# Kernel tuning notes

Hardware: AMD Instinct MI355X
Metric: run time of the kernel (lower is better)

The kernel has to match this reference:

```python
import jax, jax.numpy as jnp
import numpy as np

B, T, C, H = 4, 2048, 1024, 16
D = C // H  # head dim = 64
ROPE_BASE = 10000.0


def _rope_cache(seq_len, dim, dtype=jnp.float32):
    # torchtune-style interleaved RoPE cache
    inv_freq = 1.0 / (ROPE_BASE ** (jnp.arange(0, dim, 2, dtype=jnp.float32) / dim))
    t = jnp.arange(seq_len, dtype=jnp.float32)
    freqs = jnp.outer(t, inv_freq)  # [T, D/2]
    return jnp.cos(freqs).astype(dtype), jnp.sin(freqs).astype(dtype)


def _apply_rope(x, cos, sin):
    # x: [B, H, T, D]; rotate interleaved pairs along last dim
    x1 = x[..., 0::2]
    x2 = x[..., 1::2]
    # broadcast cos/sin [T, D/2] -> [1, 1, T, D/2]
    o1 = x1 * cos - x2 * sin
    o2 = x2 * cos + x1 * sin
    out = jnp.stack([o1, o2], axis=-1).reshape(x.shape)
    return out


def setup_inputs() -> dict:
    key = jax.random.key(0)
    k1, k2, k3 = jax.random.split(key, 3)
    x = jax.random.normal(k1, (B, T, C), dtype=jnp.float32)
    W_in = jax.random.normal(k2, (C, 3 * C), dtype=jnp.float32) * (1.0 / np.sqrt(C))
    b_in = jnp.zeros((3 * C,), dtype=jnp.float32)
    W_out = jax.random.normal(k3, (C, C), dtype=jnp.float32) * (1.0 / np.sqrt(C))
    b_out = jnp.zeros((C,), dtype=jnp.float32)
    return {"x": x, "W_in": W_in, "b_in": b_in, "W_out": W_out, "b_out": b_out}


def reference(x, W_in, b_in, W_out, b_out):
    Bx, Tx, Cx = x.shape
    qkv = x @ W_in + b_in                      # [B, T, 3C]
    q, k, v = jnp.split(qkv, 3, axis=-1)
    # [B, T, C] -> [B, H, T, D]
    def to_heads(t):
        return t.reshape(Bx, Tx, H, D).transpose(0, 2, 1, 3)
    q, k, v = to_heads(q), to_heads(k), to_heads(v)

    cos, sin = _rope_cache(Tx, D, dtype=x.dtype)
    q = _apply_rope(q, cos, sin)
    k = _apply_rope(k, cos, sin)

    scale = 1.0 / np.sqrt(D)
    att = jnp.einsum('bhqd,bhkd->bhqk', q, k) * scale   # [B, H, T, T]
    causal = jnp.tril(jnp.ones((Tx, Tx), dtype=bool))
    att = jnp.where(causal[None, None, :, :], att, jnp.float32(-jnp.inf).astype(att.dtype))
    att = jax.nn.softmax(att, axis=-1)
    # dropout = 0.0 (eval mode): identity
    y = jnp.einsum('bhqk,bhkd->bhqd', att, v)           # [B, H, T, D]
    y = y.transpose(0, 2, 1, 3).reshape(Bx, Tx, Cx)     # [B, T, C]
    return y @ W_out + b_out
```

## Files before the change

kernel.cpp:

```cpp
#include <hip/hip_runtime.h>

#define B_ 4
#define T_ 2048
#define C_ 1024
#define H_ 16
#define D_ 64
#define M_ (B_*T_)
#define N3_ (3*C_)
#define NKT_ 32

typedef unsigned short u16;
typedef short bf16x8 __attribute__((ext_vector_type(8)));
typedef short bf16x4 __attribute__((ext_vector_type(4)));
typedef unsigned short u16x8 __attribute__((ext_vector_type(8)));
typedef unsigned int u32x4 __attribute__((ext_vector_type(4)));
typedef float f32x4 __attribute__((ext_vector_type(4)));
typedef float f32x16 __attribute__((ext_vector_type(16)));

#define QSCALE 0.18033688f
#define DEFER_THR 11.0f

__device__ __forceinline__ u16 f2bf(float f) {
  unsigned u = __float_as_uint(f);
  u += 0x7fffu + ((u >> 16) & 1u);
  return (u16)(u >> 16);
}
__device__ __forceinline__ float bf2f(u16 u) { return __uint_as_float(((unsigned)u) << 16); }

__device__ __forceinline__ unsigned cvt_pk_bf16(float lo, float hi) {
  unsigned r;
  asm("v_cvt_pk_bf16_f32 %0, %1, %2" : "=v"(r) : "v"(lo), "v"(hi));
  return r;
}

__device__ __forceinline__ void gload16(const void* g, void* l) {
  __builtin_amdgcn_global_load_lds((const __attribute__((address_space(1))) void*)g,
                                   (__attribute__((address_space(3))) void*)l, 16, 0, 0);
}

__global__ __launch_bounds__(256) void k_convert(const float* __restrict__ in,
                                                 u16* __restrict__ out, int n8) {
  int i = blockIdx.x * 256 + threadIdx.x;
  if (i >= n8) return;
  f32x4 a = *(const f32x4*)(in + (size_t)i * 8);
  f32x4 b = *(const f32x4*)(in + (size_t)i * 8 + 4);
  u16x8 o;
  #pragma unroll
  for (int j = 0; j < 4; ++j) { o[j] = f2bf(a[j]); o[4 + j] = f2bf(b[j]); }
  *(u16x8*)(out + (size_t)i * 8) = o;
}

__global__ __launch_bounds__(256) void k_transpose(const float* __restrict__ W,
                                                   u16* __restrict__ Wt, int K, int N) {
  __shared__ float tile[64][65];
  int n0 = blockIdx.x * 64, k0 = blockIdx.y * 64;
  int c = threadIdx.x & 63, r0 = threadIdx.x >> 6;
  #pragma unroll
  for (int i = 0; i < 16; ++i) {
    int r = i * 4 + r0;
    tile[r][c] = W[(size_t)(k0 + r) * N + n0 + c];
  }
  __syncthreads();
  #pragma unroll
  for (int i = 0; i < 16; ++i) {
    int r = i * 4 + r0;
    Wt[(size_t)(n0 + r) * K + k0 + c] = f2bf(tile[c][r]);
  }
}

__global__ void k_rope_table(float* __restrict__ ct, float* __restrict__ st) {
  int idx = blockIdx.x * 256 + threadIdx.x;
  int t = idx >> 5, i = idx & 31;
  double inv = exp(-(2.0 * (double)i / 64.0) * log(10000.0));
  double a = (double)t * inv;
  ct[idx] = (float)cos(a);
  st[idx] = (float)sin(a);
}

__global__ __launch_bounds__(256) void k_vtrans(const u16* __restrict__ V,
                                                u16* __restrict__ Vt) {
  __shared__ u16 tile[64][65];
  int t0 = blockIdx.x * 64;
  size_t bh = (size_t)blockIdx.z * H_ + blockIdx.y;
  const u16* src = V + (bh * T_ + t0) * D_;
  u16* dst = Vt + bh * (size_t)D_ * T_ + t0;
  int r0 = threadIdx.x >> 3, c0 = (threadIdx.x & 7) * 8;
  #pragma unroll
  for (int i = 0; i < 2; ++i) {
    int rr = i * 32 + r0;
    u16x8 v = *(const u16x8*)(src + rr * D_ + c0);
    #pragma unroll
    for (int j = 0; j < 8; ++j) tile[rr][c0 + j] = v[j];
  }
  __syncthreads();
  #pragma unroll
  for (int i = 0; i < 2; ++i) {
    int d = i * 32 + r0;
    u16x8 o;
    #pragma unroll
    for (int j = 0; j < 8; ++j) o[j] = tile[c0 + j][d];
    *(u16x8*)(dst + (size_t)d * T_ + c0) = o;
  }
}

template <int MODE>
__global__ __launch_bounds__(256) void k_gemm(const u16* __restrict__ A,
                                              const u16* __restrict__ Bt,
                                              const float* __restrict__ bias,
                                              float* __restrict__ Cout,
                                              u16* __restrict__ Qb, u16* __restrict__ Kb,
                                              u16* __restrict__ Vb,
                                              const float* __restrict__ ctab,
                                              const float* __restrict__ stab,
                                              int Md, int Nd, int Kd) {
  __shared__ u16 sAB[2][128 * 64];
  u16* sA = sAB[0];
  u16* sB = sAB[1];
  const int tid = threadIdx.x, lane = tid & 63, w = tid >> 6;
  const int g = lane >> 4, r = lane & 15;
  const int wm = w >> 1, wn = w & 1;
  const int lin = blockIdx.y * gridDim.x + blockIdx.x;
  const int tM = ((lin & 7) * 8 + ((lin >> 3) & 7)) * 128;
  const int tN = (lin >> 6) * 128;

  f32x4 acc[4][4];
  #pragma unroll
  for (int i = 0; i < 4; ++i)
    #pragma unroll
    for (int j = 0; j < 4; ++j) acc[i][j] = (f32x4){0.f, 0.f, 0.f, 0.f};

  for (int k0 = 0; k0 < Kd; k0 += 64) {
    #pragma unroll
    for (int i = 0; i < 4; ++i) {
      int c = i * 256 + tid, row = c >> 3, slot = (c & 7) ^ (row & 7);
      gload16(A + (size_t)(tM + row) * Kd + k0 + slot * 8, sA + (i * 256 + w * 64) * 8);
    }
    #pragma unroll
    for (int i = 0; i < 4; ++i) {
      int c = i * 256 + tid, row = c >> 3, slot = (c & 7) ^ (row & 7);
      gload16(Bt + (size_t)(tN + row) * Kd + k0 + slot * 8, sB + (i * 256 + w * 64) * 8);
    }
    __syncthreads();
    bf16x8 af[4][2], bfr[4][2];
    #pragma unroll
    for (int mt = 0; mt < 4; ++mt)
      #pragma unroll
      for (int kk = 0; kk < 2; ++kk) {
        int row = wm * 64 + mt * 16 + r;
        af[mt][kk] = *(const bf16x8*)(sA + ((row * 64 + kk * 32 + g * 8) ^ ((row & 7) << 3)));
      }
    #pragma unroll
    for (int nt = 0; nt < 4; ++nt)
      #pragma unroll
      for (int kk = 0; kk < 2; ++kk) {
        int row = wn * 64 + nt * 16 + r;
        bfr[nt][kk] = *(const bf16x8*)(sB + ((row * 64 + kk * 32 + g * 8) ^ ((row & 7) << 3)));
      }
    __builtin_amdgcn_s_setprio(1);
    #pragma unroll
    for (int mt = 0; mt < 4; ++mt)
      #pragma unroll
      for (int nt = 0; nt < 4; ++nt)
        #pragma unroll
        for (int kk = 0; kk < 2; ++kk)
          acc[mt][nt] = __builtin_amdgcn_mfma_f32_16x16x32_bf16(af[mt][kk], bfr[nt][kk],
                                                                acc[mt][nt], 0, 0, 0);
    __builtin_amdgcn_s_setprio(0);
    __syncthreads();
  }

  if (MODE == 1) {
    #pragma unroll
    for (int mt = 0; mt < 4; ++mt)
      #pragma unroll
      for (int nt = 0; nt < 4; ++nt) {
        int n = tN + wn * 64 + nt * 16 + r;
        float bv = bias[n];
        #pragma unroll
        for (int reg = 0; reg < 4; ++reg) {
          int m = tM + wm * 64 + mt * 16 + g * 4 + reg;
          Cout[(size_t)m * Nd + n] = acc[mt][nt][reg] + bv;
        }
      }
  } else {
    u16* tile = &sAB[0][0];
    #pragma unroll
    for (int mt = 0; mt < 4; ++mt)
      #pragma unroll
      for (int nt = 0; nt < 4; ++nt) {
        int nl = wn * 64 + nt * 16 + r;
        int n = tN + nl;
        float bv = bias[n];
        int sec = n >> 10, dd = n & 63;
        #pragma unroll
        for (int reg = 0; reg < 4; ++reg) {
          int ml = wm * 64 + mt * 16 + g * 4 + reg;
          int tt = (tM + ml) & (T_ - 1);
          float v = acc[mt][nt][reg] + bv;
          if (sec < 2) {
            float pv = __shfl_xor(v, 1);
            int pi = tt * 32 + (dd >> 1);
            float c = ctab[pi], sn = stab[pi];
            v = (dd & 1) ? (v * c + pv * sn) : (v * c - pv * sn);
            if (sec == 0) v *= QSCALE;
          }
          tile[ml * 128 + ((((nl >> 3) ^ (ml & 7)) << 3) | (nl & 7))] = f2bf(v);
        }
      }
    __syncthreads();
    #pragma unroll
    for (int i = 0; i < 8; ++i) {
      int row = w * 32 + (i & 3) * 8 + (lane >> 3);
      int cc = (i >> 2) * 8 + (lane & 7);
      u16x8 val = *(const u16x8*)(tile + row * 128 + ((cc ^ (row & 7)) << 3));
      int n = tN + cc * 8;
      int m = tM + row;
      int sec = n >> 10, idx = n & 1023, hh = idx >> 6, dd = idx & 63;
      int bb = m >> 11, tt = m & (T_ - 1);
      size_t off = ((size_t)(bb * H_ + hh) * T_ + tt) * D_ + dd;
      u16* dst = sec == 0 ? Qb : (sec == 1 ? Kb : Vb);
      *(u16x8*)(dst + off) = val;
    }
  }
}

__global__ __launch_bounds__(128) void k_attn(const u16* __restrict__ Qb,
                                              const u16* __restrict__ Kb,
                                              const u16* __restrict__ Vt,
                                              u16* __restrict__ Y) {
  __shared__ u16 sK[2][64 * 64];
  __shared__ u16 sV[2][64 * 64];
  const int tid = threadIdx.x, w = tid >> 6;
  const int lane = tid & 63, col = lane & 31, hi = lane >> 5;
  const int pair = blockIdx.x;
  const int h = blockIdx.y, b = blockIdx.z;
  const size_t bhK = ((size_t)b * H_ + h) * T_;
  const size_t bhV = ((size_t)b * H_ + h) * D_;

  const int qtA = pair, qtB = (NKT_ - 1) - pair;
  const int ntA = qtA + 1;
  const int total = NKT_ + 1;

  auto STAGE = [&](int buf, int kt) {
    #pragma unroll
    for (int i = 0; i < 4; ++i) {
      int c = i * 128 + tid, row = c >> 3, slot = (c & 7) ^ (row & 7);
      gload16(Kb + (bhK + kt * 64 + row) * D_ + slot * 8, &sK[buf][(i * 128 + w * 64) * 8]);
    }
    #pragma unroll
    for (int i = 0; i < 4; ++i) {
      int c = i * 128 + tid, row = c >> 3, slot = (c & 7) ^ (row & 7);
      gload16(Vt + (bhV + row) * T_ + kt * 64 + slot * 8, &sV[buf][(i * 128 + w * 64) * 8]);
    }
  };

  int qw = qtA * 64 + w * 32;
  int tq = qw + col;
  bf16x8 qf[4];
  #pragma unroll
  for (int c = 0; c < 4; ++c)
    qf[c] = *(const bf16x8*)(Qb + (bhK + tq) * D_ + c * 16 + hi * 8);

  float m_run = -3e38f, l_run = 0.f;
  f32x16 o0, o1;
  #pragma unroll
  for (int i = 0; i < 16; ++i) { o0[i] = 0.f; o1[i] = 0.f; }

  auto FINAL = [&]() {
    float lr = l_run + __shfl_xor(l_run, 32);
    float rl = 1.0f / lr;
    u16* yrow = Y + ((size_t)b * T_ + tq) * C_ + h * 64;
    #pragma unroll
    for (int dt = 0; dt < 2; ++dt)
      #pragma unroll
      for (int j = 0; j < 8; ++j) {
        float a0 = (dt ? o1[2 * j] : o0[2 * j]) * rl;
        float a1 = (dt ? o1[2 * j + 1] : o0[2 * j + 1]) * rl;
        int d = dt * 32 + 8 * (j >> 1) + 4 * hi + 2 * (j & 1);
        *(unsigned*)(yrow + d) = cvt_pk_bf16(a0, a1);
      }
  };

  STAGE(0, 0);
  __syncthreads();

  for (int it = 0; it < total; ++it) {
    const int cur = it & 1;
    if (it + 1 < total) {
      int nit = it + 1;
      STAGE(cur ^ 1, nit < ntA ? nit : nit - ntA);
    }
    const int ktl = it < ntA ? it : it - ntA;
    const int kb = ktl * 64;
    if (kb <= qw + 31) {
      const bool act1 = (kb + 32 <= qw + 31);
      f32x16 s0, s1;
      #pragma unroll
      for (int i = 0; i < 16; ++i) { s0[i] = 0.f; s1[i] = 0.f; }

      __builtin_amdgcn_s_setprio(1);
      #pragma unroll
      for (int c = 0; c < 4; ++c) {
        int row = col;
        bf16x8 kf = *(const bf16x8*)(&sK[cur][(row * 64 + c * 16 + hi * 8) ^ ((row & 7) << 3)]);
        s0 = __builtin_amdgcn_mfma_f32_32x32x16_bf16(kf, qf[c], s0, 0, 0, 0);
      }
      if (act1) {
        #pragma unroll
        for (int c = 0; c < 4; ++c) {
          int row = 32 + col;
          bf16x8 kf = *(const bf16x8*)(&sK[cur][(row * 64 + c * 16 + hi * 8) ^ ((row & 7) << 3)]);
          s1 = __builtin_amdgcn_mfma_f32_32x32x16_bf16(kf, qf[c], s1, 0, 0, 0);
        }
      }
      __builtin_amdgcn_s_setprio(0);

      if (kb + 31 > qw) {
        #pragma unroll
        for (int reg = 0; reg < 16; ++reg) {
          int key = kb + (reg & 3) + 8 * (reg >> 2) + 4 * hi;
          if (key > tq) s0[reg] = -3e38f;
        }
      }
      if (act1 && kb + 63 > qw) {
        #pragma unroll
        for (int reg = 0; reg < 16; ++reg) {
          int key = kb + 32 + (reg & 3) + 8 * (reg >> 2) + 4 * hi;
          if (key > tq) s1[reg] = -3e38f;
        }
      }

      float pm = s0[0];
      #pragma unroll
      for (int reg = 1; reg < 16; ++reg) pm = fmaxf(pm, s0[reg]);
      if (act1) {
        #pragma unroll
        for (int reg = 0; reg < 16; ++reg) pm = fmaxf(pm, s1[reg]);
      }
      if (__any(pm > m_run + DEFER_THR)) {
        float tm = fmaxf(pm, __shfl_xor(pm, 32));
        float mn = fmaxf(m_run, tm);
        float f = __builtin_amdgcn_exp2f(m_run - mn);
        m_run = mn;
        #pragma unroll
        for (int i = 0; i < 16; ++i) { o0[i] *= f; o1[i] *= f; }
        l_run *= f;
      }

      #pragma unroll
      for (int reg = 0; reg < 16; ++reg) {
        s0[reg] = __builtin_amdgcn_exp2f(s0[reg] - m_run);
        l_run += s0[reg];
      }
      if (act1) {
        #pragma unroll
        for (int reg = 0; reg < 16; ++reg) {
          s1[reg] = __builtin_amdgcn_exp2f(s1[reg] - m_run);
          l_run += s1[reg];
        }
      }

      __builtin_amdgcn_s_setprio(1);
      #pragma unroll
      for (int st = 0; st < 2; ++st) {
        if (st == 1 && !act1) break;
        #pragma unroll
        for (int u = 0; u < 2; ++u) {
          u32x4 pw;
          #pragma unroll
          for (int j = 0; j < 4; ++j) {
            int jr = (4 * u + j) * 2;
            pw[j] = st ? cvt_pk_bf16(s1[jr], s1[jr + 1])
                       : cvt_pk_bf16(s0[jr], s0[jr + 1]);
          }
          bf16x8 pf = __builtin_bit_cast(bf16x8, pw);
          const int keybase = st * 32 + u * 16;
          #pragma unroll
          for (int dt = 0; dt < 2; ++dt) {
            int row = dt * 32 + col;
            int e0 = (row * 64 + keybase + 4 * hi) ^ ((row & 7) << 3);
            int e1 = (row * 64 + keybase + 8 + 4 * hi) ^ ((row & 7) << 3);
            bf16x4 vlo = *(const bf16x4*)(&sV[cur][e0]);
            bf16x4 vhi = *(const bf16x4*)(&sV[cur][e1]);
            bf16x8 vf;
            vf[0] = vlo[0]; vf[1] = vlo[1]; vf[2] = vlo[2]; vf[3] = vlo[3];
            vf[4] = vhi[0]; vf[5] = vhi[1]; vf[6] = vhi[2]; vf[7] = vhi[3];
            if (dt == 0) o0 = __builtin_amdgcn_mfma_f32_32x32x16_bf16(vf, pf, o0, 0, 0, 0);
            else         o1 = __builtin_amdgcn_mfma_f32_32x32x16_bf16(vf, pf, o1, 0, 0, 0);
          }
        }
      }
      __builtin_amdgcn_s_setprio(0);
    }
    __syncthreads();

    if (it == ntA - 1) {
      FINAL();
      qw = qtB * 64 + w * 32;
      tq = qw + col;
      #pragma unroll
      for (int c = 0; c < 4; ++c)
        qf[c] = *(const bf16x8*)(Qb + (bhK + tq) * D_ + c * 16 + hi * 8);
      m_run = -3e38f; l_run = 0.f;
      #pragma unroll
      for (int i = 0; i < 16; ++i) { o0[i] = 0.f; o1[i] = 0.f; }
    }
  }
  FINAL();
}

extern "C" void kernel_launch(void* const* d_in, const int* in_sizes, int n_in,
                              void* d_out, int out_size, void* d_ws, size_t ws_size,
                              hipStream_t stream) {
  const float* x     = (const float*)d_in[0];
  const float* W_in  = (const float*)d_in[1];
  const float* b_in  = (const float*)d_in[2];
  const float* W_out = (const float*)d_in[3];
  const float* b_out = (const float*)d_in[4];
  float* out = (float*)d_out;

  const size_t NE = (size_t)B_ * H_ * T_ * D_;
  u16* Qb    = (u16*)d_ws;
  u16* Kb    = Qb + NE;
  u16* Vb    = Kb + NE;
  u16* xbf   = Vb + NE;
  u16* WtIn  = xbf + (size_t)M_ * C_;
  u16* WtOut = WtIn + (size_t)N3_ * C_;
  float* ctab = (float*)(WtOut + (size_t)C_ * C_);
  float* stab = ctab + T_ * 32;
  u16* Vt  = xbf;
  u16* ybf = Vb;

  size_t needed = (size_t)((char*)(stab + T_ * 32) - (char*)d_ws);
  if (ws_size < needed) return;

  k_convert<<<4096, 256, 0, stream>>>(x, xbf, (M_ * C_) / 8);
  k_transpose<<<dim3(N3_ / 64, C_ / 64), 256, 0, stream>>>(W_in, WtIn, C_, N3_);
  k_transpose<<<dim3(C_ / 64, C_ / 64), 256, 0, stream>>>(W_out, WtOut, C_, C_);
  k_rope_table<<<(T_ * 32) / 256, 256, 0, stream>>>(ctab, stab);

  k_gemm<0><<<dim3(N3_ / 128, M_ / 128), 256, 0, stream>>>(
      xbf, WtIn, b_in, nullptr, Qb, Kb, Vb, ctab, stab, M_, N3_, C_);

  k_vtrans<<<dim3(T_ / 64, H_, B_), 256, 0, stream>>>(Vb, Vt);

  k_attn<<<dim3(NKT_ / 2, H_, B_), 128, 0, stream>>>(Qb, Kb, Vt, ybf);

  k_gemm<1><<<dim3(C_ / 128, M_ / 128), 256, 0, stream>>>(
      ybf, WtOut, b_out, out, nullptr, nullptr, nullptr, nullptr, nullptr, M_, C_, C_);
}
```

Before: 214.6 us.

## Merge prep kernels into one launch and write V transposed from QKV GEMM epilogue

Combines the x conversion, both weight transposes and the RoPE table build into a single k_prep kernel that dispatches on block index, cutting three launches. The QKV GEMM epilogue now writes the V section directly in [b,h,d,t] layout from the shared-memory tile, which removes the separate V transpose kernel and its extra read and write of V. The V-section store gathers strided u16 values from LDS, so it may hit bank conflicts and add epilogue cost. Workspace aliasing changes so that ybf reuses the xbf buffer.

```diff
diff --git a/kernel.cpp b/kernel.cpp
--- a/kernel.cpp
+++ b/kernel.cpp
@@ -38,68 +38,49 @@
                                    (__attribute__((address_space(3))) void*)l, 16, 0, 0);
 }
 
-__global__ __launch_bounds__(256) void k_convert(const float* __restrict__ in,
-                                                 u16* __restrict__ out, int n8) {
-  int i = blockIdx.x * 256 + threadIdx.x;
-  if (i >= n8) return;
-  f32x4 a = *(const f32x4*)(in + (size_t)i * 8);
-  f32x4 b = *(const f32x4*)(in + (size_t)i * 8 + 4);
-  u16x8 o;
-  #pragma unroll
-  for (int j = 0; j < 4; ++j) { o[j] = f2bf(a[j]); o[4 + j] = f2bf(b[j]); }
-  *(u16x8*)(out + (size_t)i * 8) = o;
-}
-
-__global__ __launch_bounds__(256) void k_transpose(const float* __restrict__ W,
-                                                   u16* __restrict__ Wt, int K, int N) {
+__global__ __launch_bounds__(256) void k_prep(const float* __restrict__ x,
+                                              u16* __restrict__ xbf,
+                                              const float* __restrict__ W_in,
+                                              u16* __restrict__ WtIn,
+                                              const float* __restrict__ W_out,
+                                              u16* __restrict__ WtOut,
+                                              float* __restrict__ ct,
+                                              float* __restrict__ st) {
   __shared__ float tile[64][65];
-  int n0 = blockIdx.x * 64, k0 = blockIdx.y * 64;
-  int c = threadIdx.x & 63, r0 = threadIdx.x >> 6;
-  #pragma unroll
-  for (int i = 0; i < 16; ++i) {
-    int r = i * 4 + r0;
-    tile[r][c] = W[(size_t)(k0 + r) * N + n0 + c];
-  }
-  __syncthreads();
-  #pragma unroll
-  for (int i = 0; i < 16; ++i) {
-    int r = i * 4 + r0;
-    Wt[(size_t)(n0 + r) * K + k0 + c] = f2bf(tile[c][r]);
-  }
-}
-
-__global__ void k_rope_table(float* __restrict__ ct, float* __restrict__ st) {
-  int idx = blockIdx.x * 256 + threadIdx.x;
-  int t = idx >> 5, i = idx & 31;
-  double inv = exp(-(2.0 * (double)i / 64.0) * log(10000.0));
-  double a = (double)t * inv;
-  ct[idx] = (float)cos(a);
-  st[idx] = (float)sin(a);
-}
-
-__global__ __launch_bounds__(256) void k_vtrans(const u16* __restrict__ V,
-                                                u16* __restrict__ Vt) {
-  __shared__ u16 tile[64][65];
-  int t0 = blockIdx.x * 64;
-  size_t bh = (size_t)blockIdx.z * H_ + blockIdx.y;
-  const u16* src = V + (bh * T_ + t0) * D_;
-  u16* dst = Vt + bh * (size_t)D_ * T_ + t0;
-  int r0 = threadIdx.x >> 3, c0 = (threadIdx.x & 7) * 8;
-  #pragma unroll
-  for (int i = 0; i < 2; ++i) {
-    int rr = i * 32 + r0;
-    u16x8 v = *(const u16x8*)(src + rr * D_ + c0);
-    #pragma unroll
-    for (int j = 0; j < 8; ++j) tile[rr][c0 + j] = v[j];
-  }
-  __syncthreads();
-  #pragma unroll
-  for (int i = 0; i < 2; ++i) {
-    int d = i * 32 + r0;
+  const int bx = blockIdx.x, tid = threadIdx.x;
+  if (bx < 4096) {
+    int i = bx * 256 + tid;
+    f32x4 a = *(const f32x4*)(x + (size_t)i * 8);
+    f32x4 b = *(const f32x4*)(x + (size_t)i * 8 + 4);
     u16x8 o;
     #pragma unroll
-    for (int j = 0; j < 8; ++j) o[j] = tile[c0 + j][d];
-    *(u16x8*)(dst + (size_t)d * T_ + c0) = o;
+    for (int j = 0; j < 4; ++j) { o[j] = f2bf(a[j]); o[4 + j] = f2bf(b[j]); }
+    *(u16x8*)(xbf + (size_t)i * 8) = o;
+  } else if (bx < 5120) {
+    const float* W; u16* Wt; int K = C_, N, b;
+    if (bx < 4864) { W = W_in; Wt = WtIn; N = N3_; b = bx - 4096; }
+    else           { W = W_out; Wt = WtOut; N = C_; b = bx - 4864; }
+    int ntiles = N / 64;
+    int n0 = (b % ntiles) * 64, k0 = (b / ntiles) * 64;
+    int c = tid & 63, r0 = tid >> 6;
+    #pragma unroll
+    for (int i = 0; i < 16; ++i) {
+      int r = i * 4 + r0;
+      tile[r][c] = W[(size_t)(k0 + r) * N + n0 + c];
+    }
+    __syncthreads();
+    #pragma unroll
+    for (int i = 0; i < 16; ++i) {
+      int r = i * 4 + r0;
+      Wt[(size_t)(n0 + r) * K + k0 + c] = f2bf(tile[c][r]);
+    }
+  } else {
+    int idx = (bx - 5120) * 256 + tid;
+    int t = idx >> 5, i = idx & 31;
+    double inv = exp(-(2.0 * (double)i / 64.0) * log(10000.0));
+    double a = (double)t * inv;
+    ct[idx] = (float)cos(a);
+    st[idx] = (float)sin(a);
   }
 }
 
@@ -109,7 +90,7 @@
                                               const float* __restrict__ bias,
                                               float* __restrict__ Cout,
                                               u16* __restrict__ Qb, u16* __restrict__ Kb,
-                                              u16* __restrict__ Vb,
+                                              u16* __restrict__ Vt,
                                               const float* __restrict__ ctab,
                                               const float* __restrict__ stab,
                                               int Md, int Nd, int Kd) {
@@ -183,6 +164,7 @@
         }
       }
   } else {
+    const int secb = tN >> 10;
     u16* tile = &sAB[0][0];
     #pragma unroll
     for (int mt = 0; mt < 4; ++mt)
@@ -191,35 +173,53 @@
         int nl = wn * 64 + nt * 16 + r;
         int n = tN + nl;
         float bv = bias[n];
-        int sec = n >> 10, dd = n & 63;
+        int dd = n & 63;
         #pragma unroll
         for (int reg = 0; reg < 4; ++reg) {
           int ml = wm * 64 + mt * 16 + g * 4 + reg;
           int tt = (tM + ml) & (T_ - 1);
           float v = acc[mt][nt][reg] + bv;
-          if (sec < 2) {
+          if (secb < 2) {
             float pv = __shfl_xor(v, 1);
             int pi = tt * 32 + (dd >> 1);
             float c = ctab[pi], sn = stab[pi];
             v = (dd & 1) ? (v * c + pv * sn) : (v * c - pv * sn);
-            if (sec == 0) v *= QSCALE;
+            if (secb == 0) v *= QSCALE;
           }
           tile[ml * 128 + ((((nl >> 3) ^ (ml & 7)) << 3) | (nl & 7))] = f2bf(v);
         }
       }
     __syncthreads();
-    #pragma unroll
-    for (int i = 0; i < 8; ++i) {
-      int row = w * 32 + (i & 3) * 8 + (lane >> 3);
-      int cc = (i >> 2) * 8 + (lane & 7);
-      u16x8 val = *(const u16x8*)(tile + row * 128 + ((cc ^ (row & 7)) << 3));
-      int n = tN + cc * 8;
-      int m = tM + row;
-      int sec = n >> 10, idx = n & 1023, hh = idx >> 6, dd = idx & 63;
-      int bb = m >> 11, tt = m & (T_ - 1);
-      size_t off = ((size_t)(bb * H_ + hh) * T_ + tt) * D_ + dd;
-      u16* dst = sec == 0 ? Qb : (sec == 1 ? Kb : Vb);
-      *(u16x8*)(dst + off) = val;
+    if (secb < 2) {
+      u16* dst = secb == 0 ? Qb : Kb;
+      #pragma unroll
+      for (int i = 0; i < 8; ++i) {
+        int row = w * 32 + (i & 3) * 8 + (lane >> 3);
+        int cc = (i >> 2) * 8 + (lane & 7);
+        u16x8 val = *(const u16x8*)(tile + row * 128 + ((cc ^ (row & 7)) << 3));
+        int n = tN + cc * 8;
+        int m = tM + row;
+        int hh = (n & 1023) >> 6, dd = n & 63;
+        int bb = m >> 11, tt = m & (T_ - 1);
+        *(u16x8*)(dst + ((size_t)(bb * H_ + hh) * T_ + tt) * D_ + dd) = val;
+      }
+    } else {
+      const int bb = tM >> 11, tt0 = tM & (T_ - 1);
+      #pragma unroll
+      for (int v = 0; v < 8; ++v) {
+        int idx = v * 256 + tid;
+        int nl = idx >> 4;
+        int tg = idx & 15;
+        u16x8 val;
+        #pragma unroll
+        for (int j = 0; j < 8; ++j) {
+          int ml = tg * 8 + j;
+          val[j] = tile[ml * 128 + ((((nl >> 3) ^ (ml & 7)) << 3) | (nl & 7))];
+        }
+        int n = tN + nl;
+        int hh = (n & 1023) >> 6, dd = n & 63;
+        *(u16x8*)(Vt + ((size_t)(bb * H_ + hh) * D_ + dd) * T_ + tt0 + tg * 8) = val;
+      }
     }
   }
 }
@@ -422,27 +422,21 @@
   const size_t NE = (size_t)B_ * H_ * T_ * D_;
   u16* Qb    = (u16*)d_ws;
   u16* Kb    = Qb + NE;
-  u16* Vb    = Kb + NE;
-  u16* xbf   = Vb + NE;
+  u16* Vt    = Kb + NE;
+  u16* xbf   = Vt + NE;
   u16* WtIn  = xbf + (size_t)M_ * C_;
   u16* WtOut = WtIn + (size_t)N3_ * C_;
   float* ctab = (float*)(WtOut + (size_t)C_ * C_);
   float* stab = ctab + T_ * 32;
-  u16* Vt  = xbf;
-  u16* ybf = Vb;
+  u16* ybf = xbf;
 
   size_t needed = (size_t)((char*)(stab + T_ * 32) - (char*)d_ws);
   if (ws_size < needed) return;
 
-  k_convert<<<4096, 256, 0, stream>>>(x, xbf, (M_ * C_) / 8);
-  k_transpose<<<dim3(N3_ / 64, C_ / 64), 256, 0, stream>>>(W_in, WtIn, C_, N3_);
-  k_transpose<<<dim3(C_ / 64, C_ / 64), 256, 0, stream>>>(W_out, WtOut, C_, C_);
-  k_rope_table<<<(T_ * 32) / 256, 256, 0, stream>>>(ctab, stab);
+  k_prep<<<5376, 256, 0, stream>>>(x, xbf, W_in, WtIn, W_out, WtOut, ctab, stab);
 
   k_gemm<0><<<dim3(N3_ / 128, M_ / 128), 256, 0, stream>>>(
-      xbf, WtIn, b_in, nullptr, Qb, Kb, Vb, ctab, stab, M_, N3_, C_);
-
-  k_vtrans<<<dim3(T_ / 64, H_, B_), 256, 0, stream>>>(Vb, Vt);
+      xbf, WtIn, b_in, nullptr, Qb, Kb, Vt, ctab, stab, M_, N3_, C_);
 
   k_attn<<<dim3(NKT_ / 2, H_, B_), 128, 0, stream>>>(Qb, Kb, Vt, ybf);
 
```

Result: faster. 205.7 us (-4.1%).
